# Kernel optimization log

Measured on AMD Instinct MI355X. Metric: run time of the kernel, lower is better.

## Reference

```python
import jax, jax.numpy as jnp
import numpy as np

B, L, D = 4, 2048, 1024
MD = D // 4      # memory_dim = dim // 4
K = 5            # kernel_size
DIL = 1          # dilation
EPS = 1e-6


def rmsnorm(x, w):
    return w * x * jax.lax.rsqrt(jnp.mean(x * x, axis=-1, keepdims=True) + EPS)


def setup_inputs() -> dict:
    key = jax.random.key(0)
    ks = jax.random.split(key, 16)
    n = lambda k, shape, s=0.02: jax.random.normal(k, shape, jnp.float32) * s
    return dict(
        x=jax.random.normal(ks[0], (B, L, D), jnp.float32),
        memory_state=jnp.zeros((B, MD), jnp.float32),
        norm_w=jnp.ones((D,), jnp.float32),
        dw_kernel=n(ks[1], (D, 1, K), 0.1),   # depthwise conv [O,I/g,K]
        dw_bias=jnp.zeros((D,), jnp.float32),
        pw_kernel=n(ks[2], (D, D)),           # 1x1 conv as [out,in]
        pw_bias=jnp.zeros((D,), jnp.float32),
        Win_w=n(ks[3], (MD, D)), Win_b=jnp.zeros((MD,), jnp.float32),
        Wf_w=n(ks[4], (MD, D + MD)), Wf_b=jnp.ones((MD,), jnp.float32),  # forget bias init 1.0
        Wu_w=n(ks[5], (MD, D + MD)), Wu_b=jnp.zeros((MD,), jnp.float32),
        Wo_w=n(ks[6], (D, D + MD)), Wo_b=jnp.zeros((D,), jnp.float32),
        router_w=n(ks[7], (2, D)), router_b=jnp.zeros((2,), jnp.float32),
        e0_w1=n(ks[8], (D, D)), e0_b1=jnp.zeros((D,), jnp.float32),
        e0_w2=n(ks[9], (D, D)), e0_b2=jnp.zeros((D,), jnp.float32),
        e1_w1=n(ks[10], (D, D)), e1_b1=jnp.zeros((D,), jnp.float32),
        e1_w2=n(ks[11], (D, D)), e1_b2=jnp.zeros((D,), jnp.float32),
        fnorm_w=jnp.ones((D,), jnp.float32),
        down_w=n(ks[12], (D // 4, D)), down_b=jnp.zeros((D // 4,), jnp.float32),
        up_w=n(ks[13], (D, D // 4)), up_b=jnp.zeros((D,), jnp.float32),
    )


def reference(x, memory_state, norm_w, dw_kernel, dw_bias, pw_kernel, pw_bias,
              Win_w, Win_b, Wf_w, Wf_b, Wu_w, Wu_b, Wo_w, Wo_b,
              router_w, router_b, e0_w1, e0_b1, e0_w2, e0_b2,
              e1_w1, e1_b1, e1_w2, e1_b2, fnorm_w, down_w, down_b, up_w, up_b):
    resid = x
    xn = rmsnorm(x, norm_w)                              # [B,L,D]

    # --- causal depthwise conv (left pad (K-1)*DIL == torch pad-both + slice[:L]) + pointwise ---
    P = (K - 1) * DIL
    xc = jnp.swapaxes(xn, 1, 2)                          # [B,D,L]
    xc = jax.lax.conv_general_dilated(
        xc, dw_kernel, window_strides=(1,), padding=[(P, 0)],
        rhs_dilation=(DIL,), dimension_numbers=('NCH', 'OIH', 'NCH'),
        feature_group_count=D) + dw_bias[None, :, None]
    x_conv = jnp.einsum('bdl,ed->ble', xc, pw_kernel) + pw_bias  # [B,L,D]

    # --- structured state recurrence (gated, scan over time) ---
    Wf_x, Wf_m = Wf_w[:, :D], Wf_w[:, D:]
    Wu_x, Wu_m = Wu_w[:, :D], Wu_w[:, D:]
    Wo_x, Wo_m = Wo_w[:, :D], Wo_w[:, D:]
    # precompute all x-dependent projections: [L,B,*]
    fx = jnp.einsum('bld,md->lbm', xn, Wf_x) + Wf_b
    ux = jnp.einsum('bld,md->lbm', xn, Wu_x) + Wu_b
    ox = jnp.einsum('bld,ed->lbe', xn, Wo_x) + Wo_b
    xm = jax.nn.silu(jnp.einsum('bld,md->lbm', xn, Win_w) + Win_b)
    xt = jnp.swapaxes(xn, 0, 1)                          # [L,B,D]

    def step(m, inp):
        fx_t, ux_t, ox_t, xm_t, x_t = inp
        f = jax.nn.sigmoid(fx_t + m @ Wf_m.T)
        u = jax.nn.sigmoid(ux_t + m @ Wu_m.T)
        m2 = f * m + u * xm_t
        out = x_t + ox_t + m2 @ Wo_m.T
        return m2, out

    new_mem, rec = jax.lax.scan(step, memory_state, (fx, ux, ox, xm, xt))
    x_rec = jnp.swapaxes(rec, 0, 1)                      # [B,L,D]

    y = x_conv + x_rec

    # --- enhanced gated fusion (2-expert soft MoE) ---
    r = jax.nn.softmax(y @ router_w.T + router_b, axis=-1)   # [B,L,2]
    e0 = jax.nn.silu(y @ e0_w1.T + e0_b1) @ e0_w2.T + e0_b2
    e1 = jax.nn.silu(y @ e1_w1.T + e1_b1) @ e1_w2.T + e1_b2
    y = rmsnorm(y + r[..., 0:1] * e0 + r[..., 1:2] * e1, fnorm_w)

    # --- low-rank FF (exact GELU) + residual ---
    ff = jax.nn.gelu(y @ down_w.T + down_b, approximate=False) @ up_w.T + up_b
    out = y + ff + resid
    return out, new_mem
```

## Files before the change

kernel.cpp:

```cpp
#include <hip/hip_runtime.h>
#include <hip/hip_bf16.h>

#define DD 1024
#define MDD 256
#define LL 2048
#define BB 4
#define NROWS (BB*LL)

typedef short bf16x8 __attribute__((ext_vector_type(8)));
typedef float f32x4 __attribute__((ext_vector_type(4)));

__device__ __forceinline__ short f2b(float x){
  __hip_bfloat16 h = __float2bfloat16(x);
  return *reinterpret_cast<short*>(&h);
}
__device__ __forceinline__ float b2f(short s){
  return __uint_as_float(((unsigned)(unsigned short)s) << 16);
}
__device__ __forceinline__ float frcp(float x){
#if __has_builtin(__builtin_amdgcn_rcpf)
  return __builtin_amdgcn_rcpf(x);
#else
  float r; asm("v_rcp_f32 %0, %1" : "=v"(r) : "v"(x)); return r;
#endif
}
__device__ __forceinline__ float fsigmoid(float x){
  return frcp(1.f + __expf(-x));
}
__device__ __forceinline__ float sel4(f32x4 a, int kg){
  float lo = (kg & 1) ? a[1] : a[0];
  float hi = (kg & 1) ? a[3] : a[2];
  return (kg & 2) ? hi : lo;
}

struct CvtDesc {
  const float* src; const float* src2; short* dstb; float* dstf;
  int n, cols, sld, soff, dld, mode;
};
struct CvtArgs { CvtDesc d[20]; };

__global__ __launch_bounds__(256) void cvt_all(CvtArgs a){
  int di = blockIdx.x >> 6;
  CvtDesc d = a.d[di];
  int base = (blockIdx.x & 63)*256 + threadIdx.x;
  for (int i = base; i < d.n; i += 64*256){
    int r = i / d.cols, c = i - r*d.cols;
    float v = d.src[(size_t)r*d.sld + d.soff + c];
    if (d.mode == 2) v += d.src2[i];
    if (d.mode == 0) d.dstb[(size_t)r*d.dld + c] = f2b(v);
    else             d.dstf[i] = v;
  }
}

__global__ __launch_bounds__(256) void rmsnorm_k(const float* __restrict__ x,
                                                 const float* __restrict__ w,
                                                 short* __restrict__ xn){
  int row = blockIdx.x, tid = threadIdx.x;
  const float* xr = x + (size_t)row*DD;
  float4 v = *(const float4*)&xr[tid*4];
  float ss = v.x*v.x + v.y*v.y + v.z*v.z + v.w*v.w;
  __shared__ float red[256];
  red[tid] = ss; __syncthreads();
  for (int s = 128; s > 0; s >>= 1){ if (tid < s) red[tid] += red[tid+s]; __syncthreads(); }
  float scale = rsqrtf(red[0]/(float)DD + 1e-6f);
  const float* wr = w + tid*4;
  short4 o;
  o.x = f2b(v.x*wr[0]*scale); o.y = f2b(v.y*wr[1]*scale);
  o.z = f2b(v.z*wr[2]*scale); o.w = f2b(v.w*wr[3]*scale);
  *(short4*)&xn[(size_t)row*2048 + tid*4] = o;
}

__global__ __launch_bounds__(256) void dwconv_k(const short* __restrict__ xnA,
                                                const float* __restrict__ dwk,
                                                const float* __restrict__ dwb,
                                                short* __restrict__ xcA){
  size_t i = (size_t)blockIdx.x*256 + threadIdx.x;
  int d = (int)(i & (DD-1));
  int l = (int)((i >> 10) & (LL-1));
  int b = (int)(i >> 21);
  float acc = dwb[d];
  const float* kk = dwk + d*5;
  #pragma unroll
  for (int k = 0; k < 5; ++k){
    int ll = l + k - 4;
    if (ll >= 0) acc += b2f(xnA[((size_t)(b*LL + ll))*2048 + d]) * kk[k];
  }
  xcA[((size_t)(b*LL + l))*2048 + 1024 + d] = f2b(acc);
}

template<int ACT, int OUTMODE, int PERMUTE>
__global__ __launch_bounds__(256) void gemm_bt(
    const short* __restrict__ A, const short* __restrict__ Bw,
    const float* __restrict__ bias, const float* __restrict__ add0,
    const float* __restrict__ add1, void* __restrict__ Cout, short* __restrict__ Cout2,
    int M, int N, int K, int lda, int ldb, int nbn){
  __shared__ __align__(16) short As[128*32];
  __shared__ __align__(16) short Bs[128*32];
  int bm = blockIdx.x / nbn, bn = blockIdx.x % nbn;
  int tid = threadIdx.x, lane = tid & 63, w = tid >> 6;
  int wm = (w >> 1)*64, wn = (w & 1)*64;
  const int r0 = lane & 15, kg = lane >> 4;

  f32x4 acc[4][4];
  #pragma unroll
  for (int i = 0; i < 4; ++i)
    #pragma unroll
    for (int j = 0; j < 4; ++j)
      #pragma unroll
      for (int r = 0; r < 4; ++r) acc[i][j][r] = 0.f;

  const int c0 = w*64 + lane;
  const int c1 = c0 + 256;
  const short* a0 = &A [(size_t)(bm*128 + (c0 >> 2))*lda + (c0 & 3)*8];
  const short* a1 = &A [(size_t)(bm*128 + (c1 >> 2))*lda + (c1 & 3)*8];
  const short* b0 = &Bw[(size_t)(bn*128 + (c0 >> 2))*ldb + (c0 & 3)*8];
  const short* b1 = &Bw[(size_t)(bn*128 + (c1 >> 2))*ldb + (c1 & 3)*8];

  for (int k0 = 0; k0 < K; k0 += 32){
    __builtin_amdgcn_global_load_lds((const __attribute__((address_space(1))) void*)(a0 + k0),
                                     (__attribute__((address_space(3))) void*)&As[w*512], 16, 0, 0);
    __builtin_amdgcn_global_load_lds((const __attribute__((address_space(1))) void*)(b0 + k0),
                                     (__attribute__((address_space(3))) void*)&Bs[w*512], 16, 0, 0);
    __builtin_amdgcn_global_load_lds((const __attribute__((address_space(1))) void*)(a1 + k0),
                                     (__attribute__((address_space(3))) void*)&As[2048 + w*512], 16, 0, 0);
    __builtin_amdgcn_global_load_lds((const __attribute__((address_space(1))) void*)(b1 + k0),
                                     (__attribute__((address_space(3))) void*)&Bs[2048 + w*512], 16, 0, 0);
    __syncthreads();
    bf16x8 av[4], bv[4];
    #pragma unroll
    for (int i = 0; i < 4; ++i) av[i] = *(const bf16x8*)&As[(wm + i*16 + r0)*32 + kg*8];
    #pragma unroll
    for (int j = 0; j < 4; ++j) bv[j] = *(const bf16x8*)&Bs[(wn + j*16 + r0)*32 + kg*8];
    #pragma unroll
    for (int i = 0; i < 4; ++i)
      #pragma unroll
      for (int j = 0; j < 4; ++j)
        acc[i][j] = __builtin_amdgcn_mfma_f32_16x16x32_bf16(av[i], bv[j], acc[i][j], 0, 0, 0);
    __syncthreads();
  }

  #pragma unroll
  for (int i = 0; i < 4; ++i){
    int grb = bm*128 + wm + i*16 + kg*4;
    #pragma unroll
    for (int j = 0; j < 4; ++j){
      int gc = bn*128 + wn + j*16 + r0;
      float bvv = bias ? bias[gc] : 0.f;
      #pragma unroll
      for (int r = 0; r < 4; ++r){
        int gr = grb + r;
        float v = acc[i][j][r] + bvv;
        if (ACT == 1) v = v / (1.f + __expf(-v));
        else if (ACT == 2) v = 0.5f*v*(1.f + erff(v*0.70710678118f));
        size_t orow = PERMUTE ? (size_t)((gr & 3)*LL + (gr >> 2)) : (size_t)gr;
        size_t oi = orow*(size_t)N + gc;
        if (add0) v += add0[oi];
        if (add1) v += add1[oi];
        if (OUTMODE == 0) ((float*)Cout)[oi] = v;
        else if (OUTMODE == 1) ((float*)Cout)[oi] += v;
        else if (OUTMODE == 2) ((short*)Cout)[oi] = f2b(v);
        else {
          float nv = ((float*)Cout)[oi] + v;
          ((float*)Cout)[oi] = nv;
          Cout2[oi] = f2b(nv);
        }
      }
    }
  }
}

__global__ __launch_bounds__(512) void scan_g34_k(
    const float* __restrict__ fxu, const short* __restrict__ Wfu,
    const float* __restrict__ m0, short* __restrict__ m2all, float* __restrict__ newmem,
    const short* __restrict__ A2, const short* __restrict__ B2,
    const float* __restrict__ bias2, const float* __restrict__ xres,
    float* __restrict__ ybuf){
  __shared__ __align__(16) short lds[8192];
  const int tid = threadIdx.x, lane = tid & 63, w = tid >> 6;
  const int r0 = lane & 15, kg = lane >> 4;

  if (blockIdx.x != 0){
    int bid = (int)blockIdx.x - 1;
    int bm = bid >> 3, bn = bid & 7;
    short* As = lds;
    short* Bs = lds + 4096;
    int wm = (w >> 2)*64, wn = (w & 3)*32;
    f32x4 acc[4][2];
    #pragma unroll
    for (int i = 0; i < 4; ++i)
      #pragma unroll
      for (int j = 0; j < 2; ++j)
        #pragma unroll
        for (int r = 0; r < 4; ++r) acc[i][j][r] = 0.f;

    const int c = tid;
    const short* ag = &A2[(size_t)(bm*128 + (c >> 2))*2048 + (c & 3)*8];
    const short* bg = &B2[(size_t)(bn*128 + (c >> 2))*2048 + (c & 3)*8];

    for (int k0 = 0; k0 < 2048; k0 += 32){
      __builtin_amdgcn_global_load_lds((const __attribute__((address_space(1))) void*)(ag + k0),
                                       (__attribute__((address_space(3))) void*)&As[w*512], 16, 0, 0);
      __builtin_amdgcn_global_load_lds((const __attribute__((address_space(1))) void*)(bg + k0),
                                       (__attribute__((address_space(3))) void*)&Bs[w*512], 16, 0, 0);
      __syncthreads();
      bf16x8 av[4], bv[2];
      #pragma unroll
      for (int i = 0; i < 4; ++i) av[i] = *(const bf16x8*)&As[(wm + i*16 + r0)*32 + kg*8];
      #pragma unroll
      for (int j = 0; j < 2; ++j) bv[j] = *(const bf16x8*)&Bs[(wn + j*16 + r0)*32 + kg*8];
      #pragma unroll
      for (int i = 0; i < 4; ++i)
        #pragma unroll
        for (int j = 0; j < 2; ++j)
          acc[i][j] = __builtin_amdgcn_mfma_f32_16x16x32_bf16(av[i], bv[j], acc[i][j], 0, 0, 0);
      __syncthreads();
    }
    #pragma unroll
    for (int i = 0; i < 4; ++i){
      int grb = bm*128 + wm + i*16 + kg*4;
      #pragma unroll
      for (int j = 0; j < 2; ++j){
        int gc = bn*128 + wn + j*16 + r0;
        float bvv = bias2[gc];
        #pragma unroll
        for (int r = 0; r < 4; ++r){
          size_t oi = (size_t)(grb + r)*1024 + gc;
          ybuf[oi] = acc[i][j][r] + bvv + xres[oi];
        }
      }
    }
    return;
  }

  short* mA0 = lds;
  short* mA1 = lds + 1088;
  const int j0 = w*32 + r0;

  bf16x8 bw[2][2][8];
  #pragma unroll
  for (int fu = 0; fu < 2; ++fu)
    #pragma unroll
    for (int p = 0; p < 2; ++p)
      #pragma unroll
      for (int kt = 0; kt < 8; ++kt)
        bw[fu][p][kt] = *(const bf16x8*)&Wfu[(size_t)(fu*256 + w*32 + p*16 + r0)*256 + kt*32 + kg*8];

  float m_reg0 = m0[kg*256 + j0];
  float m_reg1 = m0[kg*256 + j0 + 16];

  float cf0, cf1, cu0, cu1, xmc0, xmc1, nx0, nx1;
  {
    size_t b0 = (size_t)kg*LL*768;
    cf0 = fxu[b0 + j0];        cf1 = fxu[b0 + j0 + 16];
    cu0 = fxu[b0 + 256 + j0];  cu1 = fxu[b0 + 256 + j0 + 16];
    float tx0 = fxu[b0 + 512 + j0], tx1 = fxu[b0 + 512 + j0 + 16];
    xmc0 = tx0*fsigmoid(tx0);  xmc1 = tx1*fsigmoid(tx1);
    size_t b1 = b0 + 768;
    nx0 = fxu[b1 + 512 + j0];  nx1 = fxu[b1 + 512 + j0 + 16];
  }
  mA0[kg*272 + j0]      = f2b(m_reg0);
  mA0[kg*272 + j0 + 16] = f2b(m_reg1);
  __syncthreads();

  for (int t = 0; t < LL; ++t){
    const short* mac = (t & 1) ? mA1 : mA0;
    short*       man = (t & 1) ? mA0 : mA1;

    bf16x8 af[8];
    #pragma unroll
    for (int kt = 0; kt < 8; ++kt)
      af[kt] = *(const bf16x8*)&mac[(r0 & 3)*272 + kt*32 + kg*8];

    float xmn0 = nx0*fsigmoid(nx0);
    float xmn1 = nx1*fsigmoid(nx1);

    __builtin_amdgcn_s_setprio(1);
    f32x4 aF0 = {0.f,0.f,0.f,0.f}, aF1 = {0.f,0.f,0.f,0.f};
    f32x4 aU0 = {0.f,0.f,0.f,0.f}, aU1 = {0.f,0.f,0.f,0.f};
    #pragma unroll
    for (int kt = 0; kt < 8; ++kt){
      aF0 = __builtin_amdgcn_mfma_f32_16x16x32_bf16(af[kt], bw[0][0][kt], aF0, 0, 0, 0);
      aF1 = __builtin_amdgcn_mfma_f32_16x16x32_bf16(af[kt], bw[0][1][kt], aF1, 0, 0, 0);
      aU0 = __builtin_amdgcn_mfma_f32_16x16x32_bf16(af[kt], bw[1][0][kt], aU0, 0, 0, 0);
      aU1 = __builtin_amdgcn_mfma_f32_16x16x32_bf16(af[kt], bw[1][1][kt], aU1, 0, 0, 0);
    }
    __builtin_amdgcn_s_setprio(0);

    float gF0 = sel4(aF0, kg), gF1 = sel4(aF1, kg);
    float gU0 = sel4(aU0, kg), gU1 = sel4(aU1, kg);

    float f0 = fsigmoid(gF0 + cf0);
    float f1 = fsigmoid(gF1 + cf1);
    float u0 = fsigmoid(gU0 + cu0);
    float u1 = fsigmoid(gU1 + cu1);
    m_reg0 = f0*m_reg0 + u0*xmc0;
    m_reg1 = f1*m_reg1 + u1*xmc1;
    short mb0 = f2b(m_reg0), mb1 = f2b(m_reg1);

    m2all[(size_t)(t*4 + kg)*256 + j0]      = mb0;
    m2all[(size_t)(t*4 + kg)*256 + j0 + 16] = mb1;

    xmc0 = xmn0; xmc1 = xmn1;
    int t1 = (t + 1 < LL) ? t + 1 : t;
    int t2 = (t + 2 < LL) ? t + 2 : t;
    size_t bfu = ((size_t)kg*LL + t1)*768;
    size_t bx  = ((size_t)kg*LL + t2)*768;
    cf0 = fxu[bfu + j0];        cf1 = fxu[bfu + j0 + 16];
    cu0 = fxu[bfu + 256 + j0];  cu1 = fxu[bfu + 256 + j0 + 16];
    nx0 = fxu[bx + 512 + j0];   nx1 = fxu[bx + 512 + j0 + 16];

    man[kg*272 + j0]      = mb0;
    man[kg*272 + j0 + 16] = mb1;
    asm volatile("s_waitcnt lgkmcnt(0)" ::: "memory");
    __builtin_amdgcn_sched_barrier(0);
    __builtin_amdgcn_s_barrier();
    __builtin_amdgcn_sched_barrier(0);
  }

  newmem[kg*256 + j0]      = m_reg0;
  newmem[kg*256 + j0 + 16] = m_reg1;
}

__global__ __launch_bounds__(256) void combine_k(
    float* __restrict__ y, const short* __restrict__ e0, const short* __restrict__ e1,
    const float* __restrict__ rw, const float* __restrict__ rb,
    const float* __restrict__ fw, short* __restrict__ y2bf){
  int row = blockIdx.x, tid = threadIdx.x;
  size_t base = (size_t)row*DD + tid*4;
  float4 vy = *(const float4*)&y[base];
  short4 s0 = *(const short4*)&e0[base];
  short4 s1 = *(const short4*)&e1[base];
  float4 w0 = *(const float4*)&rw[tid*4];
  float4 w1 = *(const float4*)&rw[DD + tid*4];
  float d0 = vy.x*w0.x + vy.y*w0.y + vy.z*w0.z + vy.w*w0.w;
  float d1 = vy.x*w1.x + vy.y*w1.y + vy.z*w1.z + vy.w*w1.w;
  __shared__ float redA[256], redB[256];
  redA[tid] = d0; redB[tid] = d1; __syncthreads();
  for (int s = 128; s > 0; s >>= 1){
    if (tid < s){ redA[tid] += redA[tid+s]; redB[tid] += redB[tid+s]; }
    __syncthreads();
  }
  float l0 = redA[0] + rb[0], l1 = redB[0] + rb[1];
  float p0 = 1.f/(1.f + __expf(l1 - l0));
  float p1 = 1.f - p0;
  float c0 = vy.x + p0*b2f(s0.x) + p1*b2f(s1.x);
  float c1 = vy.y + p0*b2f(s0.y) + p1*b2f(s1.y);
  float c2 = vy.z + p0*b2f(s0.z) + p1*b2f(s1.z);
  float c3 = vy.w + p0*b2f(s0.w) + p1*b2f(s1.w);
  float ss = c0*c0 + c1*c1 + c2*c2 + c3*c3;
  __syncthreads();
  redA[tid] = ss; __syncthreads();
  for (int s = 128; s > 0; s >>= 1){
    if (tid < s) redA[tid] += redA[tid+s];
    __syncthreads();
  }
  float scale = rsqrtf(redA[0]/(float)DD + 1e-6f);
  const float* fwp = fw + tid*4;
  float o0 = c0*fwp[0]*scale, o1 = c1*fwp[1]*scale, o2 = c2*fwp[2]*scale, o3 = c3*fwp[3]*scale;
  float4 ov; ov.x = o0; ov.y = o1; ov.z = o2; ov.w = o3;
  *(float4*)&y[base] = ov;
  short4 ob; ob.x = f2b(o0); ob.y = f2b(o1); ob.z = f2b(o2); ob.w = f2b(o3);
  *(short4*)&y2bf[base] = ob;
}

extern "C" void kernel_launch(void* const* d_in, const int* in_sizes, int n_in,
                              void* d_out, int out_size, void* d_ws, size_t ws_size,
                              hipStream_t stream){
  (void)in_sizes; (void)n_in; (void)out_size; (void)ws_size;
  const float* x     = (const float*)d_in[0];
  const float* mem0  = (const float*)d_in[1];
  const float* normw = (const float*)d_in[2];
  const float* dwk   = (const float*)d_in[3];
  const float* dwb   = (const float*)d_in[4];
  const float* pw    = (const float*)d_in[5];
  const float* pwb   = (const float*)d_in[6];
  const float* Win_w = (const float*)d_in[7];
  const float* Win_b = (const float*)d_in[8];
  const float* Wf_w  = (const float*)d_in[9];
  const float* Wf_b  = (const float*)d_in[10];
  const float* Wu_w  = (const float*)d_in[11];
  const float* Wu_b  = (const float*)d_in[12];
  const float* Wo_w  = (const float*)d_in[13];
  const float* Wo_b  = (const float*)d_in[14];
  const float* rw    = (const float*)d_in[15];
  const float* rb    = (const float*)d_in[16];
  const float* e0w1  = (const float*)d_in[17];
  const float* e0b1  = (const float*)d_in[18];
  const float* e0w2  = (const float*)d_in[19];
  const float* e0b2  = (const float*)d_in[20];
  const float* e1w1  = (const float*)d_in[21];
  const float* e1b1  = (const float*)d_in[22];
  const float* e1w2  = (const float*)d_in[23];
  const float* e1b2  = (const float*)d_in[24];
  const float* fnw   = (const float*)d_in[25];
  const float* dnw   = (const float*)d_in[26];
  const float* dnb   = (const float*)d_in[27];
  const float* upw   = (const float*)d_in[28];
  const float* upb   = (const float*)d_in[29];

  char* ws = (char*)d_ws;
  size_t off = 0;
  auto alloc = [&](size_t bytes)->char*{
    char* p = ws + off; off += (bytes + 255) & ~(size_t)255; return p;
  };
  short* A2       = (short*)alloc((size_t)NROWS*2048*2);
  short* B2       = (short*)alloc((size_t)1024*2048*2);
  short* W_fxuwin = (short*)alloc((size_t)768*1024*2);
  short* W_fum    = (short*)alloc((size_t)512*256*2);
  short* W_om     = (short*)alloc((size_t)1024*256*2);
  short* W_e01    = (short*)alloc((size_t)2048*1024*2);
  short* W_e0w2   = (short*)alloc((size_t)1024*1024*2);
  short* W_e1w2   = (short*)alloc((size_t)1024*1024*2);
  short* W_down   = (short*)alloc((size_t)256*1024*2);
  short* W_up     = (short*)alloc((size_t)1024*256*2);
  float* bias768  = (float*)alloc(768*4);
  float* bias2    = (float*)alloc(1024*4);
  float* bias01   = (float*)alloc(2048*4);
  float* fxu      = (float*)alloc((size_t)NROWS*768*4);
  float* ybuf     = (float*)alloc((size_t)NROWS*DD*4);
  short* m2all    = (short*)alloc((size_t)NROWS*MDD*2);
  short* ybf      = (short*)alloc((size_t)NROWS*DD*2);
  short* e0v      = (short*)alloc((size_t)NROWS*DD*2);
  short* e1v      = (short*)alloc((size_t)NROWS*DD*2);
  short* h01      = (short*)alloc((size_t)NROWS*2048*2);
  short* hd = m2all;
  short* y2bf = ybf;
  float* y2   = ybuf;

  CvtArgs ca;
  auto D0 = [&](const float* s, short* db, int rows, int cols, int sld, int soff, int dld){
    return CvtDesc{s, nullptr, db, nullptr, rows*cols, cols, sld, soff, dld, 0};
  };
  auto D1 = [&](const float* s, float* df, int n){
    return CvtDesc{s, nullptr, nullptr, df, n, n, 0, 0, 0, 1};
  };
  ca.d[0]  = D0(Wo_w,  B2,                1024, 1024, 1280, 0,    2048);
  ca.d[1]  = D0(pw,    B2+1024,           1024, 1024, 1024, 0,    2048);
  ca.d[2]  = D0(Wf_w,  W_fxuwin,           256, 1024, 1280, 0,    1024);
  ca.d[3]  = D0(Wu_w,  W_fxuwin+256*1024,  256, 1024, 1280, 0,    1024);
  ca.d[4]  = D0(Win_w, W_fxuwin+512*1024,  256, 1024, 1024, 0,    1024);
  ca.d[5]  = D0(Wf_w,  W_fum,              256,  256, 1280, 1024, 256);
  ca.d[6]  = D0(Wu_w,  W_fum+256*256,      256,  256, 1280, 1024, 256);
  ca.d[7]  = D0(Wo_w,  W_om,              1024,  256, 1280, 1024, 256);
  ca.d[8]  = D0(e0w1,  W_e01,             1024, 1024, 1024, 0,    1024);
  ca.d[9]  = D0(e1w1,  W_e01+1024*1024,   1024, 1024, 1024, 0,    1024);
  ca.d[10] = D0(e0w2,  W_e0w2,            1024, 1024, 1024, 0,    1024);
  ca.d[11] = D0(e1w2,  W_e1w2,            1024, 1024, 1024, 0,    1024);
  ca.d[12] = D0(dnw,   W_down,             256, 1024, 1024, 0,    1024);
  ca.d[13] = D0(upw,   W_up,              1024,  256,  256, 0,    256);
  ca.d[14] = D1(Wf_b,  bias768,       256);
  ca.d[15] = D1(Wu_b,  bias768+256,   256);
  ca.d[16] = D1(Win_b, bias768+512,   256);
  ca.d[17] = CvtDesc{Wo_b, pwb, nullptr, bias2, 1024, 1024, 0, 0, 0, 2};
  ca.d[18] = D1(e0b1,  bias01,       1024);
  ca.d[19] = D1(e1b1,  bias01+1024,  1024);
  cvt_all<<<20*64, 256, 0, stream>>>(ca);

  rmsnorm_k<<<NROWS, 256, 0, stream>>>(x, normw, A2);
  dwconv_k<<<(NROWS*DD)/256, 256, 0, stream>>>(A2, dwk, dwb, A2);

  gemm_bt<0,0,0><<<64*6, 256, 0, stream>>>(A2, W_fxuwin, bias768, nullptr, nullptr,
                                           fxu, nullptr, NROWS, 768, 1024, 2048, 1024, 6);
  scan_g34_k<<<513, 512, 0, stream>>>(fxu, W_fum, mem0, m2all,
                                      (float*)d_out + (size_t)NROWS*DD,
                                      A2, B2, bias2, x, ybuf);
  gemm_bt<0,3,1><<<64*8, 256, 0, stream>>>(m2all, W_om, nullptr, nullptr, nullptr,
                                           ybuf, ybf, NROWS, 1024, 256, 256, 256, 8);
  gemm_bt<1,2,0><<<64*16, 256, 0, stream>>>(ybf, W_e01, bias01, nullptr, nullptr,
                                            h01, nullptr, NROWS, 2048, 1024, 1024, 1024, 16);
  gemm_bt<0,2,0><<<64*8, 256, 0, stream>>>(h01, W_e0w2, e0b2, nullptr, nullptr,
                                           e0v, nullptr, NROWS, 1024, 1024, 2048, 1024, 8);
  gemm_bt<0,2,0><<<64*8, 256, 0, stream>>>(h01+1024, W_e1w2, e1b2, nullptr, nullptr,
                                           e1v, nullptr, NROWS, 1024, 1024, 2048, 1024, 8);
  combine_k<<<NROWS, 256, 0, stream>>>(ybuf, e0v, e1v, rw, rb, fnw, y2bf);
  gemm_bt<2,2,0><<<64*2, 256, 0, stream>>>(y2bf, W_down, dnb, nullptr, nullptr,
                                           hd, nullptr, NROWS, 256, 1024, 1024, 1024, 2);
  gemm_bt<0,0,0><<<64*8, 256, 0, stream>>>(hd, W_up, upb, y2, x,
                                           (float*)d_out, nullptr, NROWS, 1024, 256, 256, 256, 8);
}
```

Measured before the change: 1.927 ms.

## Prefetch scan operands after barrier and merge expert down-projection GEMMs

The sequential scan loop now writes the new memory state to LDS, syncs, and immediately loads the next step's MFMA A-fragments before issuing global stores and prefetches. This shortens the serial critical path per timestep. Weight fragments are pinned in registers with empty asm, and launch bounds hint 2 waves per SIMD. The two expert second-layer GEMMs are merged into one dual launch to fill more CUs and drop a launch. Register pressure from the launch-bounds change could cause spills.

```diff
diff --git a/kernel.cpp b/kernel.cpp
--- a/kernel.cpp
+++ b/kernel.cpp
@@ -9,6 +9,7 @@
 
 typedef short bf16x8 __attribute__((ext_vector_type(8)));
 typedef float f32x4 __attribute__((ext_vector_type(4)));
+typedef int   i32x4 __attribute__((ext_vector_type(4)));
 
 __device__ __forceinline__ short f2b(float x){
   __hip_bfloat16 h = __float2bfloat16(x);
@@ -88,15 +89,20 @@
   xcA[((size_t)(b*LL + l))*2048 + 1024 + d] = f2b(acc);
 }
 
-template<int ACT, int OUTMODE, int PERMUTE>
+template<int ACT, int OUTMODE, int PERMUTE, int DUAL>
 __global__ __launch_bounds__(256) void gemm_bt(
     const short* __restrict__ A, const short* __restrict__ Bw,
     const float* __restrict__ bias, const float* __restrict__ add0,
     const float* __restrict__ add1, void* __restrict__ Cout, short* __restrict__ Cout2,
-    int M, int N, int K, int lda, int ldb, int nbn){
+    const short* A_b, const short* Bw_b, const float* bias_b, void* Cout_b,
+    int M, int N, int K, int lda, int ldb, int nbn, int nsplit){
   __shared__ __align__(16) short As[128*32];
   __shared__ __align__(16) short Bs[128*32];
-  int bm = blockIdx.x / nbn, bn = blockIdx.x % nbn;
+  int bid = blockIdx.x;
+  if (DUAL && bid >= nsplit){
+    A = A_b; Bw = Bw_b; bias = bias_b; Cout = Cout_b; bid -= nsplit;
+  }
+  int bm = bid / nbn, bn = bid % nbn;
   int tid = threadIdx.x, lane = tid & 63, w = tid >> 6;
   int wm = (w >> 1)*64, wn = (w & 1)*64;
   const int r0 = lane & 15, kg = lane >> 4;
@@ -169,7 +175,7 @@
   }
 }
 
-__global__ __launch_bounds__(512) void scan_g34_k(
+__global__ __launch_bounds__(512, 2) void scan_g34_k(
     const float* __restrict__ fxu, const short* __restrict__ Wfu,
     const float* __restrict__ m0, short* __restrict__ m2all, float* __restrict__ newmem,
     const short* __restrict__ A2, const short* __restrict__ B2,
@@ -242,8 +248,11 @@
     #pragma unroll
     for (int p = 0; p < 2; ++p)
       #pragma unroll
-      for (int kt = 0; kt < 8; ++kt)
+      for (int kt = 0; kt < 8; ++kt){
         bw[fu][p][kt] = *(const bf16x8*)&Wfu[(size_t)(fu*256 + w*32 + p*16 + r0)*256 + kt*32 + kg*8];
+        i32x4* pi = (i32x4*)&bw[fu][p][kt];
+        asm volatile("" : "+v"(*pi));
+      }
 
   float m_reg0 = m0[kg*256 + j0];
   float m_reg1 = m0[kg*256 + j0 + 16];
@@ -262,14 +271,13 @@
   mA0[kg*272 + j0 + 16] = f2b(m_reg1);
   __syncthreads();
 
+  bf16x8 af[8];
+  #pragma unroll
+  for (int kt = 0; kt < 8; ++kt)
+    af[kt] = *(const bf16x8*)&mA0[(r0 & 3)*272 + kt*32 + kg*8];
+
   for (int t = 0; t < LL; ++t){
-    const short* mac = (t & 1) ? mA1 : mA0;
-    short*       man = (t & 1) ? mA0 : mA1;
-
-    bf16x8 af[8];
-    #pragma unroll
-    for (int kt = 0; kt < 8; ++kt)
-      af[kt] = *(const bf16x8*)&mac[(r0 & 3)*272 + kt*32 + kg*8];
+    short* man = (t & 1) ? mA0 : mA1;
 
     float xmn0 = nx0*fsigmoid(nx0);
     float xmn1 = nx1*fsigmoid(nx1);
@@ -296,6 +304,20 @@
     m_reg0 = f0*m_reg0 + u0*xmc0;
     m_reg1 = f1*m_reg1 + u1*xmc1;
     short mb0 = f2b(m_reg0), mb1 = f2b(m_reg1);
+
+    man[kg*272 + j0]      = mb0;
+    man[kg*272 + j0 + 16] = mb1;
+    asm volatile("s_waitcnt lgkmcnt(0)" ::: "memory");
+    __builtin_amdgcn_sched_barrier(0);
+    __builtin_amdgcn_s_barrier();
+    __builtin_amdgcn_sched_barrier(0);
+
+    if (t + 1 < LL){
+      #pragma unroll
+      for (int kt = 0; kt < 8; ++kt)
+        af[kt] = *(const bf16x8*)&man[(r0 & 3)*272 + kt*32 + kg*8];
+    }
+    __builtin_amdgcn_sched_barrier(0);
 
     m2all[(size_t)(t*4 + kg)*256 + j0]      = mb0;
     m2all[(size_t)(t*4 + kg)*256 + j0 + 16] = mb1;
@@ -308,13 +330,6 @@
     cf0 = fxu[bfu + j0];        cf1 = fxu[bfu + j0 + 16];
     cu0 = fxu[bfu + 256 + j0];  cu1 = fxu[bfu + 256 + j0 + 16];
     nx0 = fxu[bx + 512 + j0];   nx1 = fxu[bx + 512 + j0 + 16];
-
-    man[kg*272 + j0]      = mb0;
-    man[kg*272 + j0 + 16] = mb1;
-    asm volatile("s_waitcnt lgkmcnt(0)" ::: "memory");
-    __builtin_amdgcn_sched_barrier(0);
-    __builtin_amdgcn_s_barrier();
-    __builtin_amdgcn_sched_barrier(0);
   }
 
   newmem[kg*256 + j0]      = m_reg0;
@@ -459,22 +474,27 @@
   rmsnorm_k<<<NROWS, 256, 0, stream>>>(x, normw, A2);
   dwconv_k<<<(NROWS*DD)/256, 256, 0, stream>>>(A2, dwk, dwb, A2);
 
-  gemm_bt<0,0,0><<<64*6, 256, 0, stream>>>(A2, W_fxuwin, bias768, nullptr, nullptr,
-                                           fxu, nullptr, NROWS, 768, 1024, 2048, 1024, 6);
+  gemm_bt<0,0,0,0><<<64*6, 256, 0, stream>>>(A2, W_fxuwin, bias768, nullptr, nullptr,
+                                             fxu, nullptr, nullptr, nullptr, nullptr, nullptr,
+                                             NROWS, 768, 1024, 2048, 1024, 6, 1<<30);
   scan_g34_k<<<513, 512, 0, stream>>>(fxu, W_fum, mem0, m2all,
                                       (float*)d_out + (size_t)NROWS*DD,
                                       A2, B2, bias2, x, ybuf);
-  gemm_bt<0,3,1><<<64*8, 256, 0, stream>>>(m2all, W_om, nullptr, nullptr, nullptr,
-                                           ybuf, ybf, NROWS, 1024, 256, 256, 256, 8);
-  gemm_bt<1,2,0><<<64*16, 256, 0, stream>>>(ybf, W_e01, bias01, nullptr, nullptr,
-                                            h01, nullptr, NROWS, 2048, 1024, 1024, 1024, 16);
-  gemm_bt<0,2,0><<<64*8, 256, 0, stream>>>(h01, W_e0w2, e0b2, nullptr, nullptr,
-                                           e0v, nullptr, NROWS, 1024, 1024, 2048, 1024, 8);
-  gemm_bt<0,2,0><<<64*8, 256, 0, stream>>>(h01+1024, W_e1w2, e1b2, nullptr, nullptr,
-                                           e1v, nullptr, NROWS, 1024, 1024, 2048, 1024, 8);
+  gemm_bt<0,3,1,0><<<64*8, 256, 0, stream>>>(m2all, W_om, nullptr, nullptr, nullptr,
+                                             ybuf, ybf, nullptr, nullptr, nullptr, nullptr,
+                                             NROWS, 1024, 256, 256, 256, 8, 1<<30);
+  gemm_bt<1,2,0,0><<<64*16, 256, 0, stream>>>(ybf, W_e01, bias01, nullptr, nullptr,
+                                              h01, nullptr, nullptr, nullptr, nullptr, nullptr,
+                                              NROWS, 2048, 1024, 1024, 1024, 16, 1<<30);
+  gemm_bt<0,2,0,1><<<64*16, 256, 0, stream>>>(h01, W_e0w2, e0b2, nullptr, nullptr,
+                                              e0v, nullptr,
+                                              h01+1024, W_e1w2, e1b2, e1v,
+                                              NROWS, 1024, 1024, 2048, 1024, 8, 512);
   combine_k<<<NROWS, 256, 0, stream>>>(ybuf, e0v, e1v, rw, rb, fnw, y2bf);
-  gemm_bt<2,2,0><<<64*2, 256, 0, stream>>>(y2bf, W_down, dnb, nullptr, nullptr,
-                                           hd, nullptr, NROWS, 256, 1024, 1024, 1024, 2);
-  gemm_bt<0,0,0><<<64*8, 256, 0, stream>>>(hd, W_up, upb, y2, x,
-                                           (float*)d_out, nullptr, NROWS, 1024, 256, 256, 256, 8);
-}
+  gemm_bt<2,2,0,0><<<64*2, 256, 0, stream>>>(y2bf, W_down, dnb, nullptr, nullptr,
+                                             hd, nullptr, nullptr, nullptr, nullptr, nullptr,
+                                             NROWS, 256, 1024, 1024, 1024, 2, 1<<30);
+  gemm_bt<0,0,0,0><<<64*8, 256, 0, stream>>>(hd, W_up, upb, y2, x,
+                                             (float*)d_out, nullptr, nullptr, nullptr, nullptr, nullptr,
+                                             NROWS, 1024, 256, 256, 256, 8, 1<<30);
+}
```

Result: slower. 2.487 ms (+29.1%).
